# Kernel tuning notes

Measured on AMD Instinct MI355X. Metric: run time of the kernel, lower is better.

Reference implementation:

```python
import jax, jax.numpy as jnp
import numpy as np

LDDT_THRESHOLDS = jnp.array([0.5, 1.0, 2.0, 4.0], dtype=jnp.float32)
NUCLEIC_ACID_CUTOFF = 30.0
OTHER_CUTOFF = 15.0


def _cdist(x):
    # pairwise euclidean distances, safe sqrt (zero grad on diagonal zeros)
    sq = jnp.sum(x * x, axis=-1)                      # [b, n]
    d2 = sq[:, :, None] + sq[:, None, :] - 2.0 * jnp.einsum('bic,bjc->bij', x, x)
    d2 = jnp.maximum(d2, 0.0)
    pos = d2 > 0.0
    return jnp.where(pos, jnp.sqrt(jnp.where(pos, d2, 1.0)), 0.0)


def setup_inputs() -> dict:
    key = jax.random.key(0)
    k1, k2, k3, k4, k5 = jax.random.split(key, 5)
    b, n = 2, 4096
    true_coords = jax.random.normal(k1, (b, n, 3), dtype=jnp.float32) * 10.0
    pred_coords = true_coords + jax.random.normal(k2, (b, n, 3), dtype=jnp.float32) * 1.0
    is_dna = jax.random.bernoulli(k3, 0.25, (b, n))
    is_rna = jax.random.bernoulli(k4, 0.25, (b, n))
    coords_mask = jax.random.bernoulli(k5, 0.9, (b, n))
    return {
        'pred_coords': pred_coords,
        'true_coords': true_coords,
        'is_dna': is_dna,
        'is_rna': is_rna,
        'coords_mask': coords_mask,
    }


def reference(pred_coords, true_coords, is_dna, is_rna, coords_mask):
    b, n, _ = pred_coords.shape
    pred_dists = _cdist(pred_coords)                  # [b, n, n]
    true_dists = _cdist(true_coords)                  # [b, n, n]
    dist_diff = jnp.abs(true_dists - pred_dists)      # [b, n, n]

    # sigmoid(threshold - dist_diff), averaged over the 4 thresholds
    eps = jax.nn.sigmoid(LDDT_THRESHOLDS - dist_diff[..., None]).mean(axis=-1)  # [b, n, n]

    is_nucleotide = is_dna | is_rna                   # [b, n]
    nuc_pair = is_nucleotide[:, :, None] & is_nucleotide[:, None, :]
    inclusion_radius = jnp.where(nuc_pair,
                                 true_dists < NUCLEIC_ACID_CUTOFF,
                                 true_dists < OTHER_CUTOFF)
    mask = inclusion_radius & ~jnp.eye(n, dtype=bool)[None]
    paired_coords_mask = coords_mask[:, :, None] & coords_mask[:, None, :]
    mask = mask & paired_coords_mask

    maskf = mask.astype(eps.dtype)
    num = jnp.sum(eps * maskf, axis=(-1, -2))         # [b]
    den = jnp.maximum(jnp.sum(maskf, axis=(-1, -2)), 1.0)
    lddt = num / den
    return 1.0 - lddt.mean()
```

## Files before the change

kernel.cpp:

```cpp
#include <hip/hip_runtime.h>
#include <math.h>

#define N      4096
#define BLOCK  256
#define JW     32
#define NITILE (N / BLOCK)
#define NTRI   1088
#define NQ     (JW / 4)

typedef float v4f __attribute__((ext_vector_type(4)));

#define PN0 4.0f
#define PN1 3.384183069f
#define PN2 0.750655861f
#define PN3 0.036699475f
#define PD1 1.128061023f
#define PD2 0.375327930f
#define PD3 0.036699475f
#define PD4 0.000553084f

__device__ __forceinline__ int tri_off(int t) { return 132 * t - 4 * t * t; }
__device__ __forceinline__ v4f splat(float x) { return (v4f){x, x, x, x}; }

__global__ __launch_bounds__(BLOCK, 4) void lddt_main_kernel(
    const float* __restrict__ pred, const float* __restrict__ truec,
    const int* __restrict__ is_dna, const int* __restrict__ is_rna,
    const int* __restrict__ cmask, float* __restrict__ ws)
{
    const int L     = blockIdx.x;
    const int batch = blockIdx.z;
    const int tid   = threadIdx.x;

    int itile = 0;
#pragma unroll
    for (int u = 1; u < NITILE; ++u) itile += (L >= tri_off(u)) ? 1 : 0;
    const int jseg = 8 * itile + (L - tri_off(itile));
    const bool diag = (jseg < 8 * itile + 8);

    const int i = itile * BLOCK + tid;

    const float* pb = pred  + (size_t)batch * N * 3;
    const float* tb = truec + (size_t)batch * N * 3;
    const int* dnab = is_dna + (size_t)batch * N;
    const int* rnab = is_rna + (size_t)batch * N;
    const int* cmb  = cmask  + (size_t)batch * N;

    __shared__ v4f spx[NQ], spy[NQ], spz[NQ], snw[NQ];
    __shared__ v4f stx[NQ], sty[NQ], stz[NQ], scw[NQ];
    const int j0 = jseg * JW;
    if (tid < JW) {
        const int j = j0 + tid;
        ((float*)spx)[tid] = pb[j*3+0];
        ((float*)spy)[tid] = pb[j*3+1];
        ((float*)spz)[tid] = pb[j*3+2];
        ((float*)snw)[tid] = (dnab[j] | rnab[j]) ? 675.0f : 0.0f;
        ((float*)stx)[tid] = tb[j*3+0];
        ((float*)sty)[tid] = tb[j*3+1];
        ((float*)stz)[tid] = tb[j*3+2];
        ((float*)scw)[tid] = cmb[j] ? 1.0f : 0.0f;
    }
    __syncthreads();

    const float pix = pb[i*3+0], piy = pb[i*3+1], piz = pb[i*3+2];
    const float tix = tb[i*3+0], tiy = tb[i*3+1], tiz = tb[i*3+2];
    const float inuc01 = (dnab[i] | rnab[i]) ? 1.0f : 0.0f;
    const float icm    = cmb[i] ? 1.0f : 0.0f;

    const v4f pix4 = splat(pix), piy4 = splat(piy), piz4 = splat(piz);
    const v4f tix4 = splat(tix), tiy4 = splat(tiy), tiz4 = splat(tiz);
    const v4f base = splat(225.0f);
    const v4f inuc4 = splat(inuc01);

    float num = 0.0f;
    v4f den4 = splat(0.0f);

#define PAIR4(Q, NEED_TRI)                                                     \
    {                                                                          \
        const v4f Px = spx[Q], Py = spy[Q], Pz = spz[Q], Pw = snw[Q];          \
        const v4f Tx = stx[Q], Ty = sty[Q], Tz = stz[Q], Tw = scw[Q];          \
        v4f dxp = pix4 - Px, dyp = piy4 - Py, dzp = piz4 - Pz;                 \
        v4f d2p = dxp * dxp + dyp * dyp + dzp * dzp;                           \
        v4f dxt = tix4 - Tx, dyt = tiy4 - Ty, dzt = tiz4 - Tz;                 \
        v4f d2t = dxt * dxt + dyt * dyt + dzt * dzt;                           \
        v4f dp, dt;                                                            \
        dp.x = __builtin_amdgcn_sqrtf(d2p.x); dt.x = __builtin_amdgcn_sqrtf(d2t.x); \
        dp.y = __builtin_amdgcn_sqrtf(d2p.y); dt.y = __builtin_amdgcn_sqrtf(d2t.y); \
        dp.z = __builtin_amdgcn_sqrtf(d2p.z); dt.z = __builtin_amdgcn_sqrtf(d2t.z); \
        dp.w = __builtin_amdgcn_sqrtf(d2p.w); dt.w = __builtin_amdgcn_sqrtf(d2t.w); \
        v4f dd = dt - dp;                                                      \
        v4f e;                                                                 \
        e.x = __expf(fminf(fabsf(dd.x), 10.0f));                               \
        e.y = __expf(fminf(fabsf(dd.y), 10.0f));                               \
        e.z = __expf(fminf(fabsf(dd.z), 10.0f));                               \
        e.w = __expf(fminf(fabsf(dd.w), 10.0f));                               \
        v4f NN = ((e * splat(PN3) + splat(PN2)) * e + splat(PN1)) * e + splat(PN0); \
        v4f ND = (((e * splat(PD4) + splat(PD3)) * e + splat(PD2)) * e + splat(PD1)) * e + splat(1.0f); \
        v4f cut = base + inuc4 * Pw;                                           \
        v4f m;                                                                 \
        { bool k0 = d2t.x < cut.x, k1 = d2t.y < cut.y,                         \
           k2 = d2t.z < cut.z, k3 = d2t.w < cut.w;                             \
          if (NEED_TRI) { const int jb = j0 + 4 * (Q);                         \
            k0 = k0 && (jb + 0 > i); k1 = k1 && (jb + 1 > i);                  \
            k2 = k2 && (jb + 2 > i); k3 = k3 && (jb + 3 > i); }                \
          m.x = k0 ? Tw.x : 0.0f; m.y = k1 ? Tw.y : 0.0f;                      \
          m.z = k2 ? Tw.z : 0.0f; m.w = k3 ? Tw.w : 0.0f; }                    \
        v4f t = m * NN;                                                        \
        den4 += m;                                                             \
        float na = fmaf(t.x, ND.y, t.y * ND.x);                                \
        num = fmaf(na, __builtin_amdgcn_rcpf(ND.x * ND.y), num);               \
        float nb = fmaf(t.z, ND.w, t.w * ND.z);                                \
        num = fmaf(nb, __builtin_amdgcn_rcpf(ND.z * ND.w), num);               \
    }

    if (diag) {
#pragma unroll 2
        for (int q = 0; q < NQ; ++q) PAIR4(q, true)
    } else {
#pragma unroll 2
        for (int q = 0; q < NQ; ++q) PAIR4(q, false)
    }
#undef PAIR4

    float den = den4.x + den4.y + den4.z + den4.w;

    num *= 0.5f * icm;
    den *= 2.0f * icm;

    for (int off = 32; off > 0; off >>= 1) {
        num += __shfl_down(num, off);
        den += __shfl_down(den, off);
    }
    __shared__ float rn[BLOCK / 64], rd[BLOCK / 64];
    const int wid = tid >> 6, lane = tid & 63;
    if (lane == 0) { rn[wid] = num; rd[wid] = den; }
    __syncthreads();
    if (tid == 0) {
        float tn = rn[0] + rn[1] + rn[2] + rn[3];
        float td = rd[0] + rd[1] + rd[2] + rd[3];
        const int bid = batch * NTRI + L;
        ws[bid * 2 + 0] = tn;
        ws[bid * 2 + 1] = td;
    }
}

__global__ __launch_bounds__(BLOCK) void finalize_kernel(
    const float* __restrict__ ws, float* __restrict__ out, int b)
{
    __shared__ float sn[4], sd[4];
    float acc = 0.0f;
    for (int k = 0; k < b; ++k) {
        float n = 0.0f, d = 0.0f;
        for (int p = threadIdx.x; p < NTRI; p += BLOCK) {
            n += ws[(k * NTRI + p) * 2 + 0];
            d += ws[(k * NTRI + p) * 2 + 1];
        }
        for (int off = 32; off > 0; off >>= 1) {
            n += __shfl_down(n, off);
            d += __shfl_down(d, off);
        }
        if ((threadIdx.x & 63) == 0) { sn[threadIdx.x >> 6] = n; sd[threadIdx.x >> 6] = d; }
        __syncthreads();
        if (threadIdx.x == 0) {
            float tn = sn[0] + sn[1] + sn[2] + sn[3];
            float td = sd[0] + sd[1] + sd[2] + sd[3];
            acc += tn / fmaxf(td, 1.0f);
        }
        __syncthreads();
    }
    if (threadIdx.x == 0) out[0] = 1.0f - acc / (float)b;
}

extern "C" void kernel_launch(void* const* d_in, const int* in_sizes, int n_in,
                              void* d_out, int out_size, void* d_ws, size_t ws_size,
                              hipStream_t stream) {
    const float* pred  = (const float*)d_in[0];
    const float* truec = (const float*)d_in[1];
    const int* is_dna  = (const int*)d_in[2];
    const int* is_rna  = (const int*)d_in[3];
    const int* cmask   = (const int*)d_in[4];
    float* out = (float*)d_out;
    float* ws  = (float*)d_ws;

    const int b = in_sizes[2] / N;

    dim3 grid(NTRI, 1, b);
    lddt_main_kernel<<<grid, BLOCK, 0, stream>>>(pred, truec, is_dna, is_rna, cmask, ws);
    finalize_kernel<<<1, BLOCK, 0, stream>>>(ws, out, b);
}
```

Before: 81.21 us.

## Transpose tile mapping so threads own j and loop over broadcast i

Swaps the roles of i and j in each tile. Each thread now holds one j point in registers and iterates over 32 i points, which are read directly from global memory as wave-uniform broadcast loads. This removes the shared-memory staging, the __syncthreads, and the v4f vector packing. The i-side coords mask and nucleotide flag are folded into a per-pair cutoff. The cost is scalar per-pair loads of i data, which the compiler may turn into scalar loads, plus some extra select work in the inner loop.

```diff
diff --git a/kernel.cpp b/kernel.cpp
--- a/kernel.cpp
+++ b/kernel.cpp
@@ -3,12 +3,9 @@
 
 #define N      4096
 #define BLOCK  256
-#define JW     32
-#define NITILE (N / BLOCK)
-#define NTRI   1088
-#define NQ     (JW / 4)
-
-typedef float v4f __attribute__((ext_vector_type(4)));
+#define ISEG   32
+#define NJT    (N / BLOCK)
+#define NTILE  1088
 
 #define PN0 4.0f
 #define PN1 3.384183069f
@@ -19,8 +16,7 @@
 #define PD3 0.036699475f
 #define PD4 0.000553084f
 
-__device__ __forceinline__ int tri_off(int t) { return 132 * t - 4 * t * t; }
-__device__ __forceinline__ v4f splat(float x) { return (v4f){x, x, x, x}; }
+__device__ __forceinline__ int tile_off(int J) { return 4 * J * (J + 1); }
 
 __global__ __launch_bounds__(BLOCK, 4) void lddt_main_kernel(
     const float* __restrict__ pred, const float* __restrict__ truec,
@@ -31,13 +27,14 @@
     const int batch = blockIdx.z;
     const int tid   = threadIdx.x;
 
-    int itile = 0;
+    int J = 0;
 #pragma unroll
-    for (int u = 1; u < NITILE; ++u) itile += (L >= tri_off(u)) ? 1 : 0;
-    const int jseg = 8 * itile + (L - tri_off(itile));
-    const bool diag = (jseg < 8 * itile + 8);
-
-    const int i = itile * BLOCK + tid;
+    for (int u = 1; u < NJT; ++u) J += (L >= tile_off(u)) ? 1 : 0;
+    const int S    = L - tile_off(J);
+    const bool diag = (S >= 8 * J);
+    const int i0   = S * ISEG;
+    const int j0   = J * BLOCK;
+    const int j    = j0 + tid;
 
     const float* pb = pred  + (size_t)batch * N * 3;
     const float* tb = truec + (size_t)batch * N * 3;
@@ -45,86 +42,57 @@
     const int* rnab = is_rna + (size_t)batch * N;
     const int* cmb  = cmask  + (size_t)batch * N;
 
-    __shared__ v4f spx[NQ], spy[NQ], spz[NQ], snw[NQ];
-    __shared__ v4f stx[NQ], sty[NQ], stz[NQ], scw[NQ];
-    const int j0 = jseg * JW;
-    if (tid < JW) {
-        const int j = j0 + tid;
-        ((float*)spx)[tid] = pb[j*3+0];
-        ((float*)spy)[tid] = pb[j*3+1];
-        ((float*)spz)[tid] = pb[j*3+2];
-        ((float*)snw)[tid] = (dnab[j] | rnab[j]) ? 675.0f : 0.0f;
-        ((float*)stx)[tid] = tb[j*3+0];
-        ((float*)sty)[tid] = tb[j*3+1];
-        ((float*)stz)[tid] = tb[j*3+2];
-        ((float*)scw)[tid] = cmb[j] ? 1.0f : 0.0f;
+    const float pjx = pb[j*3+0], pjy = pb[j*3+1], pjz = pb[j*3+2];
+    const float tjx = tb[j*3+0], tjy = tb[j*3+1], tjz = tb[j*3+2];
+    const float cutA = (dnab[j] | rnab[j]) ? 900.0f : 225.0f;
+    const float cjw  = cmb[j] ? 1.0f : 0.0f;
+
+    float num = 0.0f, den = 0.0f;
+
+#define IBODY(IDX, NEED_TRI, TT, NDOUT)                                        \
+    {                                                                          \
+        const int i = i0 + (IDX);                                              \
+        const float six = pb[i*3+0], siy = pb[i*3+1], siz = pb[i*3+2];         \
+        const float tix = tb[i*3+0], tiy = tb[i*3+1], tiz = tb[i*3+2];         \
+        const bool nuci = (dnab[i] | rnab[i]) != 0;                            \
+        const bool cmi  = cmb[i] != 0;                                         \
+        float dxp = pjx - six, dyp = pjy - siy, dzp = pjz - siz;               \
+        float d2p = dxp*dxp + dyp*dyp + dzp*dzp;                               \
+        float dxt = tjx - tix, dyt = tjy - tiy, dzt = tjz - tiz;               \
+        float d2t = dxt*dxt + dyt*dyt + dzt*dzt;                               \
+        float dpv = __builtin_amdgcn_sqrtf(d2p);                               \
+        float dtv = __builtin_amdgcn_sqrtf(d2t);                               \
+        float e   = __expf(fminf(fabsf(dtv - dpv), 10.0f));                    \
+        float NNv = ((e * PN3 + PN2) * e + PN1) * e + PN0;                     \
+        NDOUT = (((e * PD4 + PD3) * e + PD2) * e + PD1) * e + 1.0f;            \
+        float cutl = cmi ? (nuci ? cutA : 225.0f) : -1.0f;                     \
+        bool k = d2t < cutl;                                                   \
+        if (NEED_TRI) k = k && (j > i);                                        \
+        float m = k ? cjw : 0.0f;                                              \
+        den += m;                                                              \
+        TT = m * NNv;                                                          \
     }
-    __syncthreads();
 
-    const float pix = pb[i*3+0], piy = pb[i*3+1], piz = pb[i*3+2];
-    const float tix = tb[i*3+0], tiy = tb[i*3+1], tiz = tb[i*3+2];
-    const float inuc01 = (dnab[i] | rnab[i]) ? 1.0f : 0.0f;
-    const float icm    = cmb[i] ? 1.0f : 0.0f;
-
-    const v4f pix4 = splat(pix), piy4 = splat(piy), piz4 = splat(piz);
-    const v4f tix4 = splat(tix), tiy4 = splat(tiy), tiz4 = splat(tiz);
-    const v4f base = splat(225.0f);
-    const v4f inuc4 = splat(inuc01);
-
-    float num = 0.0f;
-    v4f den4 = splat(0.0f);
-
-#define PAIR4(Q, NEED_TRI)                                                     \
-    {                                                                          \
-        const v4f Px = spx[Q], Py = spy[Q], Pz = spz[Q], Pw = snw[Q];          \
-        const v4f Tx = stx[Q], Ty = sty[Q], Tz = stz[Q], Tw = scw[Q];          \
-        v4f dxp = pix4 - Px, dyp = piy4 - Py, dzp = piz4 - Pz;                 \
-        v4f d2p = dxp * dxp + dyp * dyp + dzp * dzp;                           \
-        v4f dxt = tix4 - Tx, dyt = tiy4 - Ty, dzt = tiz4 - Tz;                 \
-        v4f d2t = dxt * dxt + dyt * dyt + dzt * dzt;                           \
-        v4f dp, dt;                                                            \
-        dp.x = __builtin_amdgcn_sqrtf(d2p.x); dt.x = __builtin_amdgcn_sqrtf(d2t.x); \
-        dp.y = __builtin_amdgcn_sqrtf(d2p.y); dt.y = __builtin_amdgcn_sqrtf(d2t.y); \
-        dp.z = __builtin_amdgcn_sqrtf(d2p.z); dt.z = __builtin_amdgcn_sqrtf(d2t.z); \
-        dp.w = __builtin_amdgcn_sqrtf(d2p.w); dt.w = __builtin_amdgcn_sqrtf(d2t.w); \
-        v4f dd = dt - dp;                                                      \
-        v4f e;                                                                 \
-        e.x = __expf(fminf(fabsf(dd.x), 10.0f));                               \
-        e.y = __expf(fminf(fabsf(dd.y), 10.0f));                               \
-        e.z = __expf(fminf(fabsf(dd.z), 10.0f));                               \
-        e.w = __expf(fminf(fabsf(dd.w), 10.0f));                               \
-        v4f NN = ((e * splat(PN3) + splat(PN2)) * e + splat(PN1)) * e + splat(PN0); \
-        v4f ND = (((e * splat(PD4) + splat(PD3)) * e + splat(PD2)) * e + splat(PD1)) * e + splat(1.0f); \
-        v4f cut = base + inuc4 * Pw;                                           \
-        v4f m;                                                                 \
-        { bool k0 = d2t.x < cut.x, k1 = d2t.y < cut.y,                         \
-           k2 = d2t.z < cut.z, k3 = d2t.w < cut.w;                             \
-          if (NEED_TRI) { const int jb = j0 + 4 * (Q);                         \
-            k0 = k0 && (jb + 0 > i); k1 = k1 && (jb + 1 > i);                  \
-            k2 = k2 && (jb + 2 > i); k3 = k3 && (jb + 3 > i); }                \
-          m.x = k0 ? Tw.x : 0.0f; m.y = k1 ? Tw.y : 0.0f;                      \
-          m.z = k2 ? Tw.z : 0.0f; m.w = k3 ? Tw.w : 0.0f; }                    \
-        v4f t = m * NN;                                                        \
-        den4 += m;                                                             \
-        float na = fmaf(t.x, ND.y, t.y * ND.x);                                \
-        num = fmaf(na, __builtin_amdgcn_rcpf(ND.x * ND.y), num);               \
-        float nb = fmaf(t.z, ND.w, t.w * ND.z);                                \
-        num = fmaf(nb, __builtin_amdgcn_rcpf(ND.z * ND.w), num);               \
+#define ILOOP(NEED_TRI)                                                        \
+    _Pragma("unroll 2")                                                        \
+    for (int ii = 0; ii < ISEG; ii += 2) {                                     \
+        float t0, t1, nd0, nd1;                                                \
+        IBODY(ii,     NEED_TRI, t0, nd0)                                       \
+        IBODY(ii + 1, NEED_TRI, t1, nd1)                                       \
+        float na = fmaf(t0, nd1, t1 * nd0);                                    \
+        num = fmaf(na, __builtin_amdgcn_rcpf(nd0 * nd1), num);                 \
     }
 
     if (diag) {
-#pragma unroll 2
-        for (int q = 0; q < NQ; ++q) PAIR4(q, true)
+        ILOOP(true)
     } else {
-#pragma unroll 2
-        for (int q = 0; q < NQ; ++q) PAIR4(q, false)
+        ILOOP(false)
     }
-#undef PAIR4
+#undef ILOOP
+#undef IBODY
 
-    float den = den4.x + den4.y + den4.z + den4.w;
-
-    num *= 0.5f * icm;
-    den *= 2.0f * icm;
+    num *= 0.5f;
+    den *= 2.0f;
 
     for (int off = 32; off > 0; off >>= 1) {
         num += __shfl_down(num, off);
@@ -137,7 +105,7 @@
     if (tid == 0) {
         float tn = rn[0] + rn[1] + rn[2] + rn[3];
         float td = rd[0] + rd[1] + rd[2] + rd[3];
-        const int bid = batch * NTRI + L;
+        const int bid = batch * NTILE + L;
         ws[bid * 2 + 0] = tn;
         ws[bid * 2 + 1] = td;
     }
@@ -150,9 +118,9 @@
     float acc = 0.0f;
     for (int k = 0; k < b; ++k) {
         float n = 0.0f, d = 0.0f;
-        for (int p = threadIdx.x; p < NTRI; p += BLOCK) {
-            n += ws[(k * NTRI + p) * 2 + 0];
-            d += ws[(k * NTRI + p) * 2 + 1];
+        for (int p = threadIdx.x; p < NTILE; p += BLOCK) {
+            n += ws[(k * NTILE + p) * 2 + 0];
+            d += ws[(k * NTILE + p) * 2 + 1];
         }
         for (int off = 32; off > 0; off >>= 1) {
             n += __shfl_down(n, off);
@@ -183,7 +151,7 @@
 
     const int b = in_sizes[2] / N;
 
-    dim3 grid(NTRI, 1, b);
+    dim3 grid(NTILE, 1, b);
     lddt_main_kernel<<<grid, BLOCK, 0, stream>>>(pred, truec, is_dna, is_rna, cmask, ws);
     finalize_kernel<<<1, BLOCK, 0, stream>>>(ws, out, b);
 }
```

Result: no change. 82.51 us (+1.6%).
